# Kernel optimization log

Measured on AMD Instinct MI355X. Metric: run time of the kernel, lower is better.

Reference implementation:

```python
import jax, jax.numpy as jnp
import numpy as np

EPS = 1e-5


def sage_conv(x, src, dst, Wl, Wr, b, n):
    # PyG SAGEConv: out_i = W_l * mean_{j in N(i)} x_j + W_r * x_i + b
    agg = jax.ops.segment_sum(x[src], dst, num_segments=n)  # [N, d]
    deg = jax.ops.segment_sum(jnp.ones_like(src, dtype=x.dtype), dst, num_segments=n)
    agg = agg / jnp.maximum(deg, 1.0)[:, None]
    return agg @ Wl + x @ Wr + b


def setup_inputs() -> dict:
    key = jax.random.key(0)
    ks = jax.random.split(key, 12)
    N, E, D_IN, D_H, D_OUT = 50000, 600000, 128, 128, 64
    x = jax.random.normal(ks[0], (N, D_IN), dtype=jnp.float32)
    edge_index = jax.random.randint(ks[1], (2, E), 0, N, dtype=jnp.int64)
    s_in = 1.0 / np.sqrt(D_IN)
    s_h = 1.0 / np.sqrt(D_H)
    return {
        "x": x,
        "edge_index": edge_index,
        "Wl0": jax.random.normal(ks[2], (D_IN, D_H), jnp.float32) * s_in,
        "Wr0": jax.random.normal(ks[3], (D_IN, D_H), jnp.float32) * s_in,
        "b0": jnp.zeros((D_H,), jnp.float32),
        "Wl1": jax.random.normal(ks[4], (D_H, D_H), jnp.float32) * s_h,
        "Wr1": jax.random.normal(ks[5], (D_H, D_H), jnp.float32) * s_h,
        "b1": jnp.zeros((D_H,), jnp.float32),
        "Wl2": jax.random.normal(ks[6], (D_H, D_OUT), jnp.float32) * s_h,
        "Wr2": jax.random.normal(ks[7], (D_H, D_OUT), jnp.float32) * s_h,
        "b2": jnp.zeros((D_OUT,), jnp.float32),
        "gamma": jnp.ones((D_H,), jnp.float32),
        "beta": jnp.zeros((D_H,), jnp.float32),
    }


def reference(x, edge_index, Wl0, Wr0, b0, Wl1, Wr1, b1, Wl2, Wr2, b2, gamma, beta):
    n = x.shape[0]
    src, dst = edge_index[0], edge_index[1]
    residual = x  # in_channels == hidden_channels -> no residual_transform
    # layer 0: conv + relu (+ dropout as identity in eval)
    h = jax.nn.relu(sage_conv(x, src, dst, Wl0, Wr0, b0, n))
    # middle layer: conv + BN(batch stats) + relu + residual
    h = sage_conv(h, src, dst, Wl1, Wr1, b1, n)
    mu = jnp.mean(h, axis=0)
    var = jnp.var(h, axis=0)  # biased, as in torch BN normalization
    h = (h - mu) * jax.lax.rsqrt(var + EPS) * gamma + beta
    h = jax.nn.relu(h) + residual
    # output layer
    h = sage_conv(h, src, dst, Wl2, Wr2, b2, n)
    return jax.nn.log_softmax(h, axis=-1)
```

## Files before the change

kernel.cpp:

```cpp
#include <hip/hip_runtime.h>
#include <hip/hip_bf16.h>


#define WS_EPS 1e-5f

typedef unsigned short ushort_t;
typedef unsigned int uint_t;
typedef ushort_t ushort8 __attribute__((ext_vector_type(8)));
typedef ushort_t ushort4v __attribute__((ext_vector_type(4)));
typedef short short8 __attribute__((ext_vector_type(8)));
typedef float f32x4 __attribute__((ext_vector_type(4)));

__device__ __forceinline__ float bf2f(ushort_t u) {
    return __uint_as_float(((uint_t)u) << 16);
}
__device__ __forceinline__ ushort_t f2bf(float f) {
    uint_t u = __float_as_uint(f);
    u = (u + 0x7fffu + ((u >> 16) & 1u)) >> 16;
    return (ushort_t)u;
}

__global__ __launch_bounds__(256) void k_deg(const int* __restrict__ ei,
                                             int* __restrict__ deg, int E) {
    int e = blockIdx.x * 256 + threadIdx.x;
    if (e < E) atomicAdd(&deg[ei[E + e]], 1);
}

constexpr int SCHUNK = 4096;

__global__ __launch_bounds__(256) void k_scan_part(const int* __restrict__ deg,
                                                   int* __restrict__ bsum, int n) {
    int t = threadIdx.x;
    int base = blockIdx.x * SCHUNK + t * 16;
    int s = 0;
#pragma unroll
    for (int j = 0; j < 16; ++j) {
        int i = base + j;
        if (i < n) s += deg[i];
    }
#pragma unroll
    for (int d = 1; d < 64; d <<= 1) s += __shfl_xor(s, d);
    __shared__ int wt[4];
    if ((t & 63) == 0) wt[t >> 6] = s;
    __syncthreads();
    if (t == 0) bsum[blockIdx.x] = wt[0] + wt[1] + wt[2] + wt[3];
}

__global__ __launch_bounds__(64) void k_scan_bsum(const int* __restrict__ bsum,
                                                  int* __restrict__ boff,
                                                  int* __restrict__ off_n, int nb) {
    int lane = threadIdx.x;
    int carry = 0;
    for (int base = 0; base < nb; base += 64) {
        int t = base + lane;
        int v = (t < nb) ? bsum[t] : 0;
        int x = v;
#pragma unroll
        for (int d = 1; d < 64; d <<= 1) {
            int y = __shfl_up(x, d);
            if (lane >= d) x += y;
        }
        if (t < nb) boff[t] = carry + x - v;
        carry += __shfl(x, 63);
    }
    if (lane == 0) *off_n = carry;
}

__global__ __launch_bounds__(256) void k_scan_apply(const int* __restrict__ deg,
                                                    const int* __restrict__ boff,
                                                    int* __restrict__ off, int n) {
    int t = threadIdx.x;
    int lane = t & 63, wid = t >> 6;
    int base = blockIdx.x * SCHUNK + t * 16;
    int v[16];
    int s = 0;
#pragma unroll
    for (int j = 0; j < 16; ++j) {
        int i = base + j;
        v[j] = (i < n) ? deg[i] : 0;
        s += v[j];
    }
    int x = s;
#pragma unroll
    for (int d = 1; d < 64; d <<= 1) {
        int y = __shfl_up(x, d);
        if (lane >= d) x += y;
    }
    __shared__ int wtot[4];
    if (lane == 63) wtot[wid] = x;
    __syncthreads();
    int woff = 0;
    for (int wj = 0; wj < wid; ++wj) woff += wtot[wj];
    int run = boff[blockIdx.x] + woff + x - s;
#pragma unroll
    for (int j = 0; j < 16; ++j) {
        int i = base + j;
        if (i < n) off[i] = run;
        run += v[j];
    }
}

__global__ __launch_bounds__(256) void k_scatter(const int* __restrict__ ei,
                                                 const int* __restrict__ off,
                                                 int* __restrict__ cur,
                                                 int* __restrict__ csr, int E) {
    int e = blockIdx.x * 256 + threadIdx.x;
    if (e < E) {
        int d = ei[E + e];
        int s = ei[e];
        int p = atomicAdd(&cur[d], 1);
        csr[off[d] + p] = s;
    }
}

__global__ __launch_bounds__(256) void k_prep(const float* __restrict__ x,
                                              ushort_t* __restrict__ xb, int total2,
                                              int nb_cvt,
                                              const float* __restrict__ Wl0,
                                              const float* __restrict__ Wr0,
                                              const float* __restrict__ Wl1,
                                              const float* __restrict__ Wr1,
                                              const float* __restrict__ Wl2,
                                              const float* __restrict__ Wr2,
                                              ushort_t* __restrict__ wts) {
    int b = blockIdx.x;
    if (b < nb_cvt) {
        int i = b * 256 + threadIdx.x;
        if (i >= total2) return;
        float2 v = *(const float2*)&x[(size_t)i * 2];
        uint_t p = (uint_t)f2bf(v.x) | ((uint_t)f2bf(v.y) << 16);
        *(uint_t*)&xb[(size_t)i * 2] = p;
        return;
    }
    int id = (b - nb_cvt) * 256 + threadIdx.x;
    if (id >= 81920) return;
    const float* W;
    int rel, nout, base;
    if (id < 65536) {
        int m = id >> 14;
        rel = id & 16383;
        nout = 128;
        base = m << 14;
        W = (m == 0) ? Wl0 : (m == 1) ? Wr0 : (m == 2) ? Wl1 : Wr1;
    } else {
        int m = (id - 65536) >> 13;
        rel = (id - 65536) & 8191;
        nout = 64;
        base = 65536 + (m << 13);
        W = (m == 0) ? Wl2 : Wr2;
    }
    int c = rel >> 7;
    int k = rel & 127;
    wts[base + rel] = f2bf(W[(size_t)k * nout + c]);
}

template <int EPI>
__global__ __launch_bounds__(256, 3) void k_dgemm(const ushort_t* __restrict__ X1,
                                                  const ushort_t* __restrict__ W1,
                                                  const ushort_t* __restrict__ X2,
                                                  const ushort_t* __restrict__ W2,
                                                  const float* __restrict__ bias,
                                                  ushort_t* __restrict__ outp,
                                                  float* __restrict__ stats, int n) {
    constexpr int K = 128, NOUT = 128;
    const int t = threadIdx.x;
    const int lane = t & 63;
    const int r16 = lane & 15, kb = lane >> 4;
    const int gwv = blockIdx.x * 4 + (t >> 6);
    const int cq = gwv & 3;
    const int strips = (n + 15) >> 4;
    const int sstride = gridDim.x;

    const int col0 = cq * 32 + r16;
    short8 B1[2][4], B2[2][4];
#pragma unroll
    for (int fn = 0; fn < 2; ++fn)
#pragma unroll
        for (int ks = 0; ks < 4; ++ks)
            B1[fn][ks] = *(const short8*)&W1[(size_t)(col0 + fn * 16) * K + ks * 32 + kb * 8];
#pragma unroll
    for (int fn = 0; fn < 2; ++fn)
#pragma unroll
        for (int ks = 0; ks < 4; ++ks)
            B2[fn][ks] = *(const short8*)&W2[(size_t)(col0 + fn * 16) * K + ks * 32 + kb * 8];

    float bcol[2] = {bias[col0], bias[col0 + 16]};
    float ssum[2] = {0.f, 0.f}, qsum[2] = {0.f, 0.f};

    auto loadA = [&](short8* a, int s) {
        int arow = s * 16 + r16;
        bool ok = arow < n;
        size_t xo = (size_t)arow * K + kb * 8;
#pragma unroll
        for (int ks = 0; ks < 4; ++ks)
            a[ks] = ok ? *(const short8*)&X1[xo + ks * 32] : (short8)0;
#pragma unroll
        for (int ks = 0; ks < 4; ++ks)
            a[4 + ks] = ok ? *(const short8*)&X2[xo + ks * 32] : (short8)0;
    };

    auto work = [&](const short8* a, int s) {
        f32x4 acc0 = (f32x4)0.f, acc1 = (f32x4)0.f;
#pragma unroll
        for (int ks = 0; ks < 4; ++ks) {
            acc0 = __builtin_amdgcn_mfma_f32_16x16x32_bf16(a[ks], B1[0][ks], acc0, 0, 0, 0);
            acc1 = __builtin_amdgcn_mfma_f32_16x16x32_bf16(a[ks], B1[1][ks], acc1, 0, 0, 0);
        }
#pragma unroll
        for (int ks = 0; ks < 4; ++ks) {
            acc0 = __builtin_amdgcn_mfma_f32_16x16x32_bf16(a[4 + ks], B2[0][ks], acc0, 0, 0, 0);
            acc1 = __builtin_amdgcn_mfma_f32_16x16x32_bf16(a[4 + ks], B2[1][ks], acc1, 0, 0, 0);
        }
        int rb = s * 16 + kb * 4;
#pragma unroll
        for (int r = 0; r < 4; ++r) {
            int row = rb + r;
            if (row >= n) continue;
            float v0 = acc0[r] + bcol[0];
            float v1 = acc1[r] + bcol[1];
            if constexpr (EPI == 2) {
                outp[(size_t)row * NOUT + col0] = f2bf(fmaxf(v0, 0.f));
                outp[(size_t)row * NOUT + col0 + 16] = f2bf(fmaxf(v1, 0.f));
            } else {
                outp[(size_t)row * NOUT + col0] = f2bf(v0);
                outp[(size_t)row * NOUT + col0 + 16] = f2bf(v1);
                ssum[0] += v0; qsum[0] += v0 * v0;
                ssum[1] += v1; qsum[1] += v1 * v1;
            }
        }
    };

    short8 aA[8], aB[8];
    int s = gwv >> 2;
    if (s < strips) {
        loadA(aA, s);
        for (;;) {
            int s1 = s + sstride;
            bool v1 = (s1 < strips);
            if (v1) loadA(aB, s1);
            work(aA, s);
            if (!v1) break;
            int s2 = s1 + sstride;
            bool v2 = (s2 < strips);
            if (v2) loadA(aA, s2);
            work(aB, s1);
            if (!v2) break;
            s = s2;
        }
    }

    if constexpr (EPI == 1) {
#pragma unroll
        for (int fn = 0; fn < 2; ++fn) {
            ssum[fn] += __shfl_xor(ssum[fn], 16);
            ssum[fn] += __shfl_xor(ssum[fn], 32);
            qsum[fn] += __shfl_xor(qsum[fn], 16);
            qsum[fn] += __shfl_xor(qsum[fn], 32);
        }
        if (kb == 0) {
#pragma unroll
            for (int fn = 0; fn < 2; ++fn) {
                atomicAdd(&stats[col0 + fn * 16], ssum[fn]);
                atomicAdd(&stats[128 + col0 + fn * 16], qsum[fn]);
            }
        }
    }
}

__global__ __launch_bounds__(256, 3) void k_cgemm(const ushort_t* __restrict__ H,
                                                  const ushort_t* __restrict__ WL,
                                                  const ushort_t* __restrict__ WR,
                                                  const float* __restrict__ b2,
                                                  ushort_t* __restrict__ A64,
                                                  float* __restrict__ T, int n) {
    constexpr int K = 128;
    const int t = threadIdx.x;
    const int lane = t & 63;
    const int r16 = lane & 15, kb = lane >> 4;
    const int gwv = blockIdx.x * 4 + (t >> 6);
    const int hf = gwv & 1;
    const int strips = (n + 15) >> 4;
    const int sstride = gridDim.x * 2;

    const int col0 = hf * 32 + r16;
    short8 BL[2][4], BR[2][4];
#pragma unroll
    for (int fn = 0; fn < 2; ++fn)
#pragma unroll
        for (int ks = 0; ks < 4; ++ks)
            BL[fn][ks] = *(const short8*)&WL[(size_t)(col0 + fn * 16) * K + ks * 32 + kb * 8];
#pragma unroll
    for (int fn = 0; fn < 2; ++fn)
#pragma unroll
        for (int ks = 0; ks < 4; ++ks)
            BR[fn][ks] = *(const short8*)&WR[(size_t)(col0 + fn * 16) * K + ks * 32 + kb * 8];

    float bcol[2] = {b2[col0], b2[col0 + 16]};

    auto loadA = [&](short8* a, int s) {
        int arow = s * 16 + r16;
        bool ok = arow < n;
        size_t xo = (size_t)arow * K + kb * 8;
#pragma unroll
        for (int ks = 0; ks < 4; ++ks)
            a[ks] = ok ? *(const short8*)&H[xo + ks * 32] : (short8)0;
    };

    auto work = [&](const short8* a, int s) {
        f32x4 al0 = (f32x4)0.f, al1 = (f32x4)0.f;
        f32x4 ar0 = (f32x4)0.f, ar1 = (f32x4)0.f;
#pragma unroll
        for (int ks = 0; ks < 4; ++ks) {
            al0 = __builtin_amdgcn_mfma_f32_16x16x32_bf16(a[ks], BL[0][ks], al0, 0, 0, 0);
            al1 = __builtin_amdgcn_mfma_f32_16x16x32_bf16(a[ks], BL[1][ks], al1, 0, 0, 0);
            ar0 = __builtin_amdgcn_mfma_f32_16x16x32_bf16(a[ks], BR[0][ks], ar0, 0, 0, 0);
            ar1 = __builtin_amdgcn_mfma_f32_16x16x32_bf16(a[ks], BR[1][ks], ar1, 0, 0, 0);
        }
        int rb = s * 16 + kb * 4;
#pragma unroll
        for (int r = 0; r < 4; ++r) {
            int row = rb + r;
            if (row >= n) continue;
            A64[(size_t)row * 64 + col0] = f2bf(al0[r]);
            A64[(size_t)row * 64 + col0 + 16] = f2bf(al1[r]);
            T[(size_t)row * 64 + col0] = ar0[r] + bcol[0];
            T[(size_t)row * 64 + col0 + 16] = ar1[r] + bcol[1];
        }
    };

    short8 aA[4], aB[4];
    int s = gwv >> 1;
    if (s < strips) {
        loadA(aA, s);
        for (;;) {
            int s1 = s + sstride;
            bool v1 = (s1 < strips);
            if (v1) loadA(aB, s1);
            work(aA, s);
            if (!v1) break;
            int s2 = s1 + sstride;
            bool v2 = (s2 < strips);
            if (v2) loadA(aA, s2);
            work(aB, s1);
            if (!v2) break;
            s = s2;
        }
    }
}

__global__ __launch_bounds__(256) void k_lsm(const float* __restrict__ T,
                                             const ushort_t* __restrict__ B64,
                                             float* __restrict__ out, int n) {
    const int t = threadIdx.x;
    const int lane = t & 63;
    const int wv = blockIdx.x * 4 + (t >> 6);
    const int row = wv * 4 + (lane >> 4);
    const int cg = lane & 15;
    const bool ok = (row < n);
    float v[4];
    if (ok) {
        f32x4 tv = *(const f32x4*)&T[(size_t)row * 64 + cg * 4];
        ushort4v bv = *(const ushort4v*)&B64[(size_t)row * 64 + cg * 4];
#pragma unroll
        for (int j = 0; j < 4; ++j) v[j] = tv[j] + bf2f((ushort_t)bv[j]);
    } else {
#pragma unroll
        for (int j = 0; j < 4; ++j) v[j] = 0.f;
    }
    float m = fmaxf(fmaxf(v[0], v[1]), fmaxf(v[2], v[3]));
#pragma unroll
    for (int d = 1; d < 16; d <<= 1) m = fmaxf(m, __shfl_xor(m, d));
    float e = expf(v[0] - m) + expf(v[1] - m) + expf(v[2] - m) + expf(v[3] - m);
#pragma unroll
    for (int d = 1; d < 16; d <<= 1) e += __shfl_xor(e, d);
    float lg = m + logf(e);
    if (ok) {
        f32x4 o;
#pragma unroll
        for (int j = 0; j < 4; ++j) o[j] = v[j] - lg;
        *(f32x4*)&out[(size_t)row * 64 + cg * 4] = o;
    }
}

template <int D>
__global__ __launch_bounds__(256) void k_segmean_bf(const ushort_t* __restrict__ U,
                                                    const int* __restrict__ off,
                                                    const int* __restrict__ srcs,
                                                    ushort_t* __restrict__ out,
                                                    int n) {
    constexpr int L = D / 8;
    constexpr int PER = 256 / L;
    int node = blockIdx.x * PER + threadIdx.x / L;
    int sub = threadIdx.x % L;
    if (node >= n) return;
    int beg = off[node], end = off[node + 1];
    float a[8];
#pragma unroll
    for (int j = 0; j < 8; ++j) a[j] = 0.f;
    int i = beg;
    for (; i + 8 <= end; i += 8) {
        int sv[8];
#pragma unroll
        for (int u = 0; u < 8; ++u) sv[u] = srcs[i + u];
#pragma unroll
        for (int u = 0; u < 8; ++u) {
            ushort8 v = *(const ushort8*)&U[(size_t)sv[u] * D + sub * 8];
#pragma unroll
            for (int j = 0; j < 8; ++j) a[j] += bf2f((ushort_t)v[j]);
        }
    }
    for (; i + 4 <= end; i += 4) {
        int sv[4];
#pragma unroll
        for (int u = 0; u < 4; ++u) sv[u] = srcs[i + u];
#pragma unroll
        for (int u = 0; u < 4; ++u) {
            ushort8 v = *(const ushort8*)&U[(size_t)sv[u] * D + sub * 8];
#pragma unroll
            for (int j = 0; j < 8; ++j) a[j] += bf2f((ushort_t)v[j]);
        }
    }
    for (; i < end; ++i) {
        ushort8 v = *(const ushort8*)&U[(size_t)srcs[i] * D + sub * 8];
#pragma unroll
        for (int j = 0; j < 8; ++j) a[j] += bf2f((ushort_t)v[j]);
    }
    int d = end - beg;
    float inv = 1.f / (float)(d > 1 ? d : 1);
    ushort8 o;
#pragma unroll
    for (int j = 0; j < 8; ++j) o[j] = f2bf(a[j] * inv);
    *(ushort8*)&out[(size_t)node * D + sub * 8] = o;
}

__global__ __launch_bounds__(256) void k_bnapply(const ushort_t* __restrict__ P,
                                                 const float* __restrict__ X,
                                                 const float* __restrict__ stats,
                                                 const float* __restrict__ gamma,
                                                 const float* __restrict__ beta,
                                                 ushort_t* __restrict__ H, int n) {
    int i = blockIdx.x * 256 + threadIdx.x;
    if (i >= n * 64) return;
    int nd = i >> 6;
    int c = (i & 63) << 1;
    float inv_n = 1.f / (float)n;
    float mu0 = stats[c] * inv_n, mu1 = stats[c + 1] * inv_n;
    float v0 = stats[128 + c] * inv_n - mu0 * mu0;
    float v1 = stats[128 + c + 1] * inv_n - mu1 * mu1;
    float s0 = rsqrtf(v0 + WS_EPS) * gamma[c];
    float s1 = rsqrtf(v1 + WS_EPS) * gamma[c + 1];
    uint_t pv = *(const uint_t*)&P[(size_t)nd * 128 + c];
    float p0 = __uint_as_float(pv << 16);
    float p1 = __uint_as_float(pv & 0xffff0000u);
    float2 xr = *(const float2*)&X[(size_t)nd * 128 + c];
    float h0 = fmaxf((p0 - mu0) * s0 + beta[c], 0.f) + xr.x;
    float h1 = fmaxf((p1 - mu1) * s1 + beta[c + 1], 0.f) + xr.y;
    uint_t pk = (uint_t)f2bf(h0) | ((uint_t)f2bf(h1) << 16);
    *(uint_t*)&H[(size_t)nd * 128 + c] = pk;
}

extern "C" void kernel_launch(void* const* d_in, const int* in_sizes, int n_in,
                              void* d_out, int out_size, void* d_ws, size_t ws_size,
                              hipStream_t stream) {
    const float* x     = (const float*)d_in[0];
    const int*   ei    = (const int*)d_in[1];
    const float* Wl0   = (const float*)d_in[2];
    const float* Wr0   = (const float*)d_in[3];
    const float* b0    = (const float*)d_in[4];
    const float* Wl1   = (const float*)d_in[5];
    const float* Wr1   = (const float*)d_in[6];
    const float* b1    = (const float*)d_in[7];
    const float* Wl2   = (const float*)d_in[8];
    const float* Wr2   = (const float*)d_in[9];
    const float* b2    = (const float*)d_in[10];
    const float* gamma = (const float*)d_in[11];
    const float* beta  = (const float*)d_in[12];

    const int n = in_sizes[0] / 128;
    const int E = in_sizes[1] / 2;
    const int nb_scan = (n + SCHUNK - 1) / SCHUNK;

    char* w = (char*)d_ws;
    auto alloc = [&](size_t bytes) -> void* {
        void* p = (void*)w;
        w += (bytes + 255) & ~(size_t)255;
        return p;
    };
    int*      deg   = (int*)alloc((size_t)n * 4);
    int*      cur   = (int*)alloc((size_t)n * 4);
    float*    stats = (float*)alloc(256 * 4);
    size_t    zbytes = (size_t)((char*)w - (char*)deg);
    int*      off   = (int*)alloc(((size_t)n + 1) * 4);
    int*      csr   = (int*)alloc((size_t)E * 4);
    int*      bsum  = (int*)alloc(256 * 4);
    int*      boff  = (int*)alloc(256 * 4);
    ushort_t* wts   = (ushort_t*)alloc((size_t)81920 * 2);
    ushort_t* xb    = (ushort_t*)alloc((size_t)n * 128 * 2);
    ushort_t* H     = (ushort_t*)alloc((size_t)n * 128 * 2);
    ushort_t* Pb    = (ushort_t*)alloc((size_t)n * 128 * 2);
    ushort_t* slabB = (ushort_t*)alloc((size_t)n * 128 * 2);
    float*    T     = (float*)alloc((size_t)n * 64 * 4);

    ushort_t* WtL0 = wts;
    ushort_t* WtR0 = wts + 16384;
    ushort_t* WtL1 = wts + 32768;
    ushort_t* WtR1 = wts + 49152;
    ushort_t* WtL2 = wts + 65536;
    ushort_t* WtR2 = wts + 73728;

    ushort_t* M   = slabB;
    ushort_t* A64 = slabB;
    ushort_t* B64 = slabB + (size_t)n * 64;

    hipMemsetAsync(deg, 0, zbytes, stream);

    const int eb = (E + 255) / 256;
    k_deg<<<eb, 256, 0, stream>>>(ei, deg, E);
    k_scan_part<<<nb_scan, 256, 0, stream>>>(deg, bsum, n);
    k_scan_bsum<<<1, 64, 0, stream>>>(bsum, boff, off + n, nb_scan);
    k_scan_apply<<<nb_scan, 256, 0, stream>>>(deg, boff, off, n);
    k_scatter<<<eb, 256, 0, stream>>>(ei, off, cur, csr, E);

    const int nb_cvt = (n * 64 + 255) / 256;
    k_prep<<<nb_cvt + 320, 256, 0, stream>>>(x, xb, n * 64, nb_cvt,
                                             Wl0, Wr0, Wl1, Wr1, Wl2, Wr2, wts);

    const int NB_G = 640;
    const int smb128 = (n + 15) / 16;
    const int smb64 = (n + 31) / 32;
    const int lsb = (n + 15) / 16;

    k_segmean_bf<128><<<smb128, 256, 0, stream>>>(xb, off, csr, M, n);
    k_dgemm<2><<<NB_G, 256, 0, stream>>>(xb, WtR0, M, WtL0, b0, H, nullptr, n);

    k_segmean_bf<128><<<smb128, 256, 0, stream>>>(H, off, csr, M, n);
    k_dgemm<1><<<NB_G, 256, 0, stream>>>(H, WtR1, M, WtL1, b1, Pb, stats, n);
    k_bnapply<<<(n * 64 + 255) / 256, 256, 0, stream>>>(Pb, x, stats, gamma, beta, H, n);

    k_cgemm<<<NB_G, 256, 0, stream>>>(H, WtL2, WtR2, b2, A64, T, n);
    k_segmean_bf<64><<<smb64, 256, 0, stream>>>(A64, off, csr, B64, n);
    k_lsm<<<lsb, 256, 0, stream>>>(T, B64, (float*)d_out, n);
}
```

Measured before the change: 234.2 us.

## Gather FP8 neighbor features, stage weights in LDS, fuse final aggregation with log-softmax

Several changes are made at once. Layer-0 and layer-1 activations get an extra 8-bit e4m3-like copy, and the neighbor-mean gathers read it and accumulate in fp16 to halve gather bandwidth. The GEMMs now load weights into shared memory with padded rows, compute 64 columns per block with triple-buffered A strips, and store the final T term in bf16. The degree count is merged into the prep kernel, the residual reads bf16 x, and the last segment-mean is fused with log-softmax. The FP8 quantization and fp16 accumulation lose precision compared with the bf16/fp32 path, which risks accuracy tolerance failures.

```diff
diff --git a/kernel.cpp b/kernel.cpp
--- a/kernel.cpp
+++ b/kernel.cpp
@@ -6,10 +6,11 @@
 
 typedef unsigned short ushort_t;
 typedef unsigned int uint_t;
+typedef unsigned char uchar_t;
 typedef ushort_t ushort8 __attribute__((ext_vector_type(8)));
-typedef ushort_t ushort4v __attribute__((ext_vector_type(4)));
 typedef short short8 __attribute__((ext_vector_type(8)));
 typedef float f32x4 __attribute__((ext_vector_type(4)));
+typedef _Float16 half2v __attribute__((ext_vector_type(2)));
 
 __device__ __forceinline__ float bf2f(ushort_t u) {
     return __uint_as_float(((uint_t)u) << 16);
@@ -19,11 +20,16 @@
     u = (u + 0x7fffu + ((u >> 16) & 1u)) >> 16;
     return (ushort_t)u;
 }
-
-__global__ __launch_bounds__(256) void k_deg(const int* __restrict__ ei,
-                                             int* __restrict__ deg, int E) {
-    int e = blockIdx.x * 256 + threadIdx.x;
-    if (e < E) atomicAdd(&deg[ei[E + e]], 1);
+__device__ __forceinline__ uchar_t f2e4m3(float f) {
+    _Float16 hf = (_Float16)f;
+    uint_t h = (uint_t)__builtin_bit_cast(unsigned short, hf);
+    uint_t s = (h >> 8) & 0x80u;
+    uint_t r = h & 0x7fffu;
+    if (r < 0x2400u) return (uchar_t)0;
+    if (r > 0x5F40u) r = 0x5F00u;
+    uint_t u = r - 0x2000u;
+    uint_t m = (u + 0x3fu + ((u >> 7) & 1u)) >> 7;
+    return (uchar_t)(s | m);
 }
 
 constexpr int SCHUNK = 4096;
@@ -113,23 +119,34 @@
     }
 }
 
-__global__ __launch_bounds__(256) void k_prep(const float* __restrict__ x,
-                                              ushort_t* __restrict__ xb, int total2,
-                                              int nb_cvt,
-                                              const float* __restrict__ Wl0,
-                                              const float* __restrict__ Wr0,
-                                              const float* __restrict__ Wl1,
-                                              const float* __restrict__ Wr1,
-                                              const float* __restrict__ Wl2,
-                                              const float* __restrict__ Wr2,
-                                              ushort_t* __restrict__ wts) {
+__global__ __launch_bounds__(256) void k_deg_prep(const int* __restrict__ ei,
+                                                  int* __restrict__ deg, int E, int eb,
+                                                  const float* __restrict__ x,
+                                                  ushort_t* __restrict__ xb,
+                                                  uchar_t* __restrict__ x8,
+                                                  int total2, int nb_cvt,
+                                                  const float* __restrict__ Wl0,
+                                                  const float* __restrict__ Wr0,
+                                                  const float* __restrict__ Wl1,
+                                                  const float* __restrict__ Wr1,
+                                                  const float* __restrict__ Wl2,
+                                                  const float* __restrict__ Wr2,
+                                                  ushort_t* __restrict__ wts) {
     int b = blockIdx.x;
+    if (b < eb) {
+        int e = b * 256 + threadIdx.x;
+        if (e < E) atomicAdd(&deg[ei[E + e]], 1);
+        return;
+    }
+    b -= eb;
     if (b < nb_cvt) {
         int i = b * 256 + threadIdx.x;
         if (i >= total2) return;
         float2 v = *(const float2*)&x[(size_t)i * 2];
         uint_t p = (uint_t)f2bf(v.x) | ((uint_t)f2bf(v.y) << 16);
         *(uint_t*)&xb[(size_t)i * 2] = p;
+        ushort_t q = (ushort_t)((uint_t)f2e4m3(v.x) | ((uint_t)f2e4m3(v.y) << 8));
+        *(ushort_t*)&x8[(size_t)i * 2] = q;
         return;
     }
     int id = (b - nb_cvt) * 256 + threadIdx.x;
@@ -154,38 +171,44 @@
     wts[base + rel] = f2bf(W[(size_t)k * nout + c]);
 }
 
+constexpr int LDK = 136;
+
 template <int EPI>
-__global__ __launch_bounds__(256, 3) void k_dgemm(const ushort_t* __restrict__ X1,
+__global__ __launch_bounds__(256, 2) void k_dgemm(const ushort_t* __restrict__ X1,
                                                   const ushort_t* __restrict__ W1,
                                                   const ushort_t* __restrict__ X2,
                                                   const ushort_t* __restrict__ W2,
                                                   const float* __restrict__ bias,
                                                   ushort_t* __restrict__ outp,
+                                                  uchar_t* __restrict__ out8,
                                                   float* __restrict__ stats, int n) {
     constexpr int K = 128, NOUT = 128;
+    __shared__ ushort_t Bs[2 * 64 * LDK];
+
     const int t = threadIdx.x;
     const int lane = t & 63;
     const int r16 = lane & 15, kb = lane >> 4;
-    const int gwv = blockIdx.x * 4 + (t >> 6);
-    const int cq = gwv & 3;
+    const int colbase = (blockIdx.x & 1) * 64;
+
+#pragma unroll
+    for (int u = 0; u < 8; ++u) {
+        int f = u * 256 + t;
+        int rel = f & 1023;
+        int col = rel >> 4, seg = rel & 15;
+        const ushort_t* Wm = (u < 4) ? W1 : W2;
+        *(ushort8*)&Bs[(u < 4 ? 0 : 1) * 64 * LDK + col * LDK + seg * 8] =
+            *(const ushort8*)&Wm[(size_t)(colbase + col) * K + seg * 8];
+    }
+    __syncthreads();
+
+    float bcol[4];
+#pragma unroll
+    for (int fn = 0; fn < 4; ++fn) bcol[fn] = bias[colbase + fn * 16 + r16];
+    float ssum[4] = {0.f, 0.f, 0.f, 0.f}, qsum[4] = {0.f, 0.f, 0.f, 0.f};
+
     const int strips = (n + 15) >> 4;
-    const int sstride = gridDim.x;
-
-    const int col0 = cq * 32 + r16;
-    short8 B1[2][4], B2[2][4];
-#pragma unroll
-    for (int fn = 0; fn < 2; ++fn)
-#pragma unroll
-        for (int ks = 0; ks < 4; ++ks)
-            B1[fn][ks] = *(const short8*)&W1[(size_t)(col0 + fn * 16) * K + ks * 32 + kb * 8];
-#pragma unroll
-    for (int fn = 0; fn < 2; ++fn)
-#pragma unroll
-        for (int ks = 0; ks < 4; ++ks)
-            B2[fn][ks] = *(const short8*)&W2[(size_t)(col0 + fn * 16) * K + ks * 32 + kb * 8];
-
-    float bcol[2] = {bias[col0], bias[col0 + 16]};
-    float ssum[2] = {0.f, 0.f}, qsum[2] = {0.f, 0.f};
+    const int wstr = (gridDim.x >> 1) * 4;
+    const int s0 = (blockIdx.x >> 1) * 4 + (t >> 6);
 
     auto loadA = [&](short8* a, int s) {
         int arow = s * 16 + r16;
@@ -200,58 +223,77 @@
     };
 
     auto work = [&](const short8* a, int s) {
-        f32x4 acc0 = (f32x4)0.f, acc1 = (f32x4)0.f;
+        f32x4 acc[4] = {(f32x4)0.f, (f32x4)0.f, (f32x4)0.f, (f32x4)0.f};
 #pragma unroll
         for (int ks = 0; ks < 4; ++ks) {
-            acc0 = __builtin_amdgcn_mfma_f32_16x16x32_bf16(a[ks], B1[0][ks], acc0, 0, 0, 0);
-            acc1 = __builtin_amdgcn_mfma_f32_16x16x32_bf16(a[ks], B1[1][ks], acc1, 0, 0, 0);
+#pragma unroll
+            for (int fn = 0; fn < 4; ++fn) {
+                short8 b = *(const short8*)&Bs[(fn * 16 + r16) * LDK + ks * 32 + kb * 8];
+                acc[fn] = __builtin_amdgcn_mfma_f32_16x16x32_bf16(a[ks], b, acc[fn], 0, 0, 0);
+            }
         }
 #pragma unroll
         for (int ks = 0; ks < 4; ++ks) {
-            acc0 = __builtin_amdgcn_mfma_f32_16x16x32_bf16(a[4 + ks], B2[0][ks], acc0, 0, 0, 0);
-            acc1 = __builtin_amdgcn_mfma_f32_16x16x32_bf16(a[4 + ks], B2[1][ks], acc1, 0, 0, 0);
+#pragma unroll
+            for (int fn = 0; fn < 4; ++fn) {
+                short8 b = *(const short8*)&Bs[64 * LDK + (fn * 16 + r16) * LDK + ks * 32 + kb * 8];
+                acc[fn] = __builtin_amdgcn_mfma_f32_16x16x32_bf16(a[4 + ks], b, acc[fn], 0, 0, 0);
+            }
         }
         int rb = s * 16 + kb * 4;
 #pragma unroll
         for (int r = 0; r < 4; ++r) {
             int row = rb + r;
             if (row >= n) continue;
-            float v0 = acc0[r] + bcol[0];
-            float v1 = acc1[r] + bcol[1];
-            if constexpr (EPI == 2) {
-                outp[(size_t)row * NOUT + col0] = f2bf(fmaxf(v0, 0.f));
-                outp[(size_t)row * NOUT + col0 + 16] = f2bf(fmaxf(v1, 0.f));
-            } else {
-                outp[(size_t)row * NOUT + col0] = f2bf(v0);
-                outp[(size_t)row * NOUT + col0 + 16] = f2bf(v1);
-                ssum[0] += v0; qsum[0] += v0 * v0;
-                ssum[1] += v1; qsum[1] += v1 * v1;
+#pragma unroll
+            for (int fn = 0; fn < 4; ++fn) {
+                int col = colbase + fn * 16 + r16;
+                float v = acc[fn][r] + bcol[fn];
+                if constexpr (EPI == 2) {
+                    float rv = fmaxf(v, 0.f);
+                    outp[(size_t)row * NOUT + col] = f2bf(rv);
+                    out8[(size_t)row * NOUT + col] = f2e4m3(rv);
+                } else {
+                    outp[(size_t)row * NOUT + col] = f2bf(v);
+                    ssum[fn] += v;
+                    qsum[fn] += v * v;
+                }
             }
         }
     };
 
-    short8 aA[8], aB[8];
-    int s = gwv >> 2;
+    short8 aA[8], aB[8], aC[8];
+    int s = s0;
     if (s < strips) {
         loadA(aA, s);
+        int sB = s + wstr;
+        bool vB = sB < strips;
+        if (vB) loadA(aB, sB);
         for (;;) {
-            int s1 = s + sstride;
-            bool v1 = (s1 < strips);
-            if (v1) loadA(aB, s1);
+            int sC = sB + wstr;
+            bool vC = vB && (sC < strips);
+            if (vC) loadA(aC, sC);
             work(aA, s);
-            if (!v1) break;
-            int s2 = s1 + sstride;
-            bool v2 = (s2 < strips);
-            if (v2) loadA(aA, s2);
-            work(aB, s1);
-            if (!v2) break;
-            s = s2;
+            if (!vB) break;
+            int sD = sC + wstr;
+            bool vD = vC && (sD < strips);
+            if (vD) loadA(aA, sD);
+            work(aB, sB);
+            if (!vC) break;
+            int sE = sD + wstr;
+            bool vE = vD && (sE < strips);
+            if (vE) loadA(aB, sE);
+            work(aC, sC);
+            if (!vD) break;
+            s = sD;
+            sB = sE;
+            vB = vE;
         }
     }
 
     if constexpr (EPI == 1) {
 #pragma unroll
-        for (int fn = 0; fn < 2; ++fn) {
+        for (int fn = 0; fn < 4; ++fn) {
             ssum[fn] += __shfl_xor(ssum[fn], 16);
             ssum[fn] += __shfl_xor(ssum[fn], 32);
             qsum[fn] += __shfl_xor(qsum[fn], 16);
@@ -259,43 +301,46 @@
         }
         if (kb == 0) {
 #pragma unroll
-            for (int fn = 0; fn < 2; ++fn) {
-                atomicAdd(&stats[col0 + fn * 16], ssum[fn]);
-                atomicAdd(&stats[128 + col0 + fn * 16], qsum[fn]);
+            for (int fn = 0; fn < 4; ++fn) {
+                int col = colbase + fn * 16 + r16;
+                atomicAdd(&stats[col], ssum[fn]);
+                atomicAdd(&stats[128 + col], qsum[fn]);
             }
         }
     }
 }
 
-__global__ __launch_bounds__(256, 3) void k_cgemm(const ushort_t* __restrict__ H,
+__global__ __launch_bounds__(256, 2) void k_cgemm(const ushort_t* __restrict__ H,
                                                   const ushort_t* __restrict__ WL,
                                                   const ushort_t* __restrict__ WR,
                                                   const float* __restrict__ b2,
                                                   ushort_t* __restrict__ A64,
-                                                  float* __restrict__ T, int n) {
+                                                  ushort_t* __restrict__ Tb, int n) {
     constexpr int K = 128;
+    __shared__ ushort_t Bs[2 * 64 * LDK];
+
     const int t = threadIdx.x;
     const int lane = t & 63;
     const int r16 = lane & 15, kb = lane >> 4;
-    const int gwv = blockIdx.x * 4 + (t >> 6);
-    const int hf = gwv & 1;
+
+#pragma unroll
+    for (int u = 0; u < 8; ++u) {
+        int f = u * 256 + t;
+        int rel = f & 1023;
+        int col = rel >> 4, seg = rel & 15;
+        const ushort_t* Wm = (u < 4) ? WL : WR;
+        *(ushort8*)&Bs[(u < 4 ? 0 : 1) * 64 * LDK + col * LDK + seg * 8] =
+            *(const ushort8*)&Wm[(size_t)col * K + seg * 8];
+    }
+    __syncthreads();
+
+    float bcol[4];
+#pragma unroll
+    for (int fn = 0; fn < 4; ++fn) bcol[fn] = b2[fn * 16 + r16];
+
     const int strips = (n + 15) >> 4;
-    const int sstride = gridDim.x * 2;
-
-    const int col0 = hf * 32 + r16;
-    short8 BL[2][4], BR[2][4];
-#pragma unroll
-    for (int fn = 0; fn < 2; ++fn)
-#pragma unroll
-        for (int ks = 0; ks < 4; ++ks)
-            BL[fn][ks] = *(const short8*)&WL[(size_t)(col0 + fn * 16) * K + ks * 32 + kb * 8];
-#pragma unroll
-    for (int fn = 0; fn < 2; ++fn)
-#pragma unroll
-        for (int ks = 0; ks < 4; ++ks)
-            BR[fn][ks] = *(const short8*)&WR[(size_t)(col0 + fn * 16) * K + ks * 32 + kb * 8];
-
-    float bcol[2] = {b2[col0], b2[col0 + 16]};
+    const int wstr = gridDim.x * 4;
+    const int s0 = blockIdx.x * 4 + (t >> 6);
 
     auto loadA = [&](short8* a, int s) {
         int arow = s * 16 + r16;
@@ -307,91 +352,128 @@
     };
 
     auto work = [&](const short8* a, int s) {
-        f32x4 al0 = (f32x4)0.f, al1 = (f32x4)0.f;
-        f32x4 ar0 = (f32x4)0.f, ar1 = (f32x4)0.f;
+        f32x4 aL[4] = {(f32x4)0.f, (f32x4)0.f, (f32x4)0.f, (f32x4)0.f};
+        f32x4 aR[4] = {(f32x4)0.f, (f32x4)0.f, (f32x4)0.f, (f32x4)0.f};
 #pragma unroll
         for (int ks = 0; ks < 4; ++ks) {
-            al0 = __builtin_amdgcn_mfma_f32_16x16x32_bf16(a[ks], BL[0][ks], al0, 0, 0, 0);
-            al1 = __builtin_amdgcn_mfma_f32_16x16x32_bf16(a[ks], BL[1][ks], al1, 0, 0, 0);
-            ar0 = __builtin_amdgcn_mfma_f32_16x16x32_bf16(a[ks], BR[0][ks], ar0, 0, 0, 0);
-            ar1 = __builtin_amdgcn_mfma_f32_16x16x32_bf16(a[ks], BR[1][ks], ar1, 0, 0, 0);
+#pragma unroll
+            for (int fn = 0; fn < 4; ++fn) {
+                short8 bl = *(const short8*)&Bs[(fn * 16 + r16) * LDK + ks * 32 + kb * 8];
+                short8 br = *(const short8*)&Bs[64 * LDK + (fn * 16 + r16) * LDK + ks * 32 + kb * 8];
+                aL[fn] = __builtin_amdgcn_mfma_f32_16x16x32_bf16(a[ks], bl, aL[fn], 0, 0, 0);
+                aR[fn] = __builtin_amdgcn_mfma_f32_16x16x32_bf16(a[ks], br, aR[fn], 0, 0, 0);
+            }
         }
         int rb = s * 16 + kb * 4;
 #pragma unroll
         for (int r = 0; r < 4; ++r) {
             int row = rb + r;
             if (row >= n) continue;
-            A64[(size_t)row * 64 + col0] = f2bf(al0[r]);
-            A64[(size_t)row * 64 + col0 + 16] = f2bf(al1[r]);
-            T[(size_t)row * 64 + col0] = ar0[r] + bcol[0];
-            T[(size_t)row * 64 + col0 + 16] = ar1[r] + bcol[1];
+#pragma unroll
+            for (int fn = 0; fn < 4; ++fn) {
+                int col = fn * 16 + r16;
+                A64[(size_t)row * 64 + col] = f2bf(aL[fn][r]);
+                Tb[(size_t)row * 64 + col] = f2bf(aR[fn][r] + bcol[fn]);
+            }
         }
     };
 
-    short8 aA[4], aB[4];
-    int s = gwv >> 1;
+    short8 aA[4], aB[4], aC[4];
+    int s = s0;
     if (s < strips) {
         loadA(aA, s);
+        int sB = s + wstr;
+        bool vB = sB < strips;
+        if (vB) loadA(aB, sB);
         for (;;) {
-            int s1 = s + sstride;
-            bool v1 = (s1 < strips);
-            if (v1) loadA(aB, s1);
+            int sC = sB + wstr;
+            bool vC = vB && (sC < strips);
+            if (vC) loadA(aC, sC);
             work(aA, s);
-            if (!v1) break;
-            int s2 = s1 + sstride;
-            bool v2 = (s2 < strips);
-            if (v2) loadA(aA, s2);
-            work(aB, s1);
-            if (!v2) break;
-            s = s2;
-        }
-    }
-}
-
-__global__ __launch_bounds__(256) void k_lsm(const float* __restrict__ T,
-                                             const ushort_t* __restrict__ B64,
-                                             float* __restrict__ out, int n) {
-    const int t = threadIdx.x;
-    const int lane = t & 63;
-    const int wv = blockIdx.x * 4 + (t >> 6);
-    const int row = wv * 4 + (lane >> 4);
-    const int cg = lane & 15;
-    const bool ok = (row < n);
-    float v[4];
-    if (ok) {
-        f32x4 tv = *(const f32x4*)&T[(size_t)row * 64 + cg * 4];
-        ushort4v bv = *(const ushort4v*)&B64[(size_t)row * 64 + cg * 4];
-#pragma unroll
-        for (int j = 0; j < 4; ++j) v[j] = tv[j] + bf2f((ushort_t)bv[j]);
-    } else {
-#pragma unroll
-        for (int j = 0; j < 4; ++j) v[j] = 0.f;
-    }
-    float m = fmaxf(fmaxf(v[0], v[1]), fmaxf(v[2], v[3]));
-#pragma unroll
-    for (int d = 1; d < 16; d <<= 1) m = fmaxf(m, __shfl_xor(m, d));
-    float e = expf(v[0] - m) + expf(v[1] - m) + expf(v[2] - m) + expf(v[3] - m);
-#pragma unroll
-    for (int d = 1; d < 16; d <<= 1) e += __shfl_xor(e, d);
-    float lg = m + logf(e);
-    if (ok) {
-        f32x4 o;
-#pragma unroll
-        for (int j = 0; j < 4; ++j) o[j] = v[j] - lg;
-        *(f32x4*)&out[(size_t)row * 64 + cg * 4] = o;
-    }
-}
-
-template <int D>
-__global__ __launch_bounds__(256) void k_segmean_bf(const ushort_t* __restrict__ U,
-                                                    const int* __restrict__ off,
-                                                    const int* __restrict__ srcs,
-                                                    ushort_t* __restrict__ out,
-                                                    int n) {
-    constexpr int L = D / 8;
-    constexpr int PER = 256 / L;
-    int node = blockIdx.x * PER + threadIdx.x / L;
-    int sub = threadIdx.x % L;
+            if (!vB) break;
+            int sD = sC + wstr;
+            bool vD = vC && (sD < strips);
+            if (vD) loadA(aA, sD);
+            work(aB, sB);
+            if (!vC) break;
+            int sE = sD + wstr;
+            bool vE = vD && (sE < strips);
+            if (vE) loadA(aB, sE);
+            work(aC, sC);
+            if (!vD) break;
+            s = sD;
+            sB = sE;
+            vB = vE;
+        }
+    }
+}
+
+__global__ __launch_bounds__(256) void k_segmean8(const uchar_t* __restrict__ U8,
+                                                  const int* __restrict__ off,
+                                                  const int* __restrict__ srcs,
+                                                  ushort_t* __restrict__ out, int n) {
+    int node = blockIdx.x * 32 + (threadIdx.x >> 3);
+    int sub = threadIdx.x & 7;
+    if (node >= n) return;
+    int beg = off[node], end = off[node + 1];
+    half2v aE0 = (half2v)0, aE1 = (half2v)0, aE2 = (half2v)0, aE3 = (half2v)0;
+    half2v aO0 = (half2v)0, aO1 = (half2v)0, aO2 = (half2v)0, aO3 = (half2v)0;
+
+#define DEC(dw, AE, AO)                                                           \
+    {                                                                             \
+        uint_t xe = (dw)&0x00ff00ffu;                                             \
+        uint_t xo = ((dw) >> 8) & 0x00ff00ffu;                                    \
+        uint_t he = ((xe & 0x00800080u) << 8) |                                   \
+                    (((xe & 0x007f007fu) << 7) + 0x20002000u);                    \
+        uint_t ho = ((xo & 0x00800080u) << 8) |                                   \
+                    (((xo & 0x007f007fu) << 7) + 0x20002000u);                    \
+        AE += __builtin_bit_cast(half2v, he);                                     \
+        AO += __builtin_bit_cast(half2v, ho);                                     \
+    }
+
+    auto addrow = [&](int sidx) {
+        uint4 v = *(const uint4*)&U8[(size_t)sidx * 128 + sub * 16];
+        DEC(v.x, aE0, aO0)
+        DEC(v.y, aE1, aO1)
+        DEC(v.z, aE2, aO2)
+        DEC(v.w, aE3, aO3)
+    };
+#undef DEC
+
+    int i = beg;
+    for (; i + 8 <= end; i += 8) {
+        int sv[8];
+#pragma unroll
+        for (int u = 0; u < 8; ++u) sv[u] = srcs[i + u];
+#pragma unroll
+        for (int u = 0; u < 8; ++u) addrow(sv[u]);
+    }
+    for (; i < end; ++i) addrow(srcs[i]);
+
+    int d = end - beg;
+    float inv = 1.f / (float)(d > 1 ? d : 1);
+    ushort8 o0, o1;
+#define PACK(AE, AO, O, IDX)                     \
+    O[IDX] = f2bf((float)AE[0] * inv);           \
+    O[IDX + 1] = f2bf((float)AO[0] * inv);       \
+    O[IDX + 2] = f2bf((float)AE[1] * inv);       \
+    O[IDX + 3] = f2bf((float)AO[1] * inv);
+    PACK(aE0, aO0, o0, 0)
+    PACK(aE1, aO1, o0, 4)
+    PACK(aE2, aO2, o1, 0)
+    PACK(aE3, aO3, o1, 4)
+#undef PACK
+    *(ushort8*)&out[(size_t)node * 128 + sub * 16] = o0;
+    *(ushort8*)&out[(size_t)node * 128 + sub * 16 + 8] = o1;
+}
+
+__global__ __launch_bounds__(256) void k_segmean_lsm(const ushort_t* __restrict__ A64,
+                                                     const int* __restrict__ off,
+                                                     const int* __restrict__ srcs,
+                                                     const ushort_t* __restrict__ Tb,
+                                                     float* __restrict__ out, int n) {
+    int node = blockIdx.x * 32 + (threadIdx.x >> 3);
+    int sub = threadIdx.x & 7;
     if (node >= n) return;
     int beg = off[node], end = off[node + 1];
     float a[8];
@@ -404,37 +486,45 @@
         for (int u = 0; u < 8; ++u) sv[u] = srcs[i + u];
 #pragma unroll
         for (int u = 0; u < 8; ++u) {
-            ushort8 v = *(const ushort8*)&U[(size_t)sv[u] * D + sub * 8];
+            ushort8 v = *(const ushort8*)&A64[(size_t)sv[u] * 64 + sub * 8];
 #pragma unroll
             for (int j = 0; j < 8; ++j) a[j] += bf2f((ushort_t)v[j]);
         }
     }
-    for (; i + 4 <= end; i += 4) {
-        int sv[4];
-#pragma unroll
-        for (int u = 0; u < 4; ++u) sv[u] = srcs[i + u];
-#pragma unroll
-        for (int u = 0; u < 4; ++u) {
-            ushort8 v = *(const ushort8*)&U[(size_t)sv[u] * D + sub * 8];
-#pragma unroll
-            for (int j = 0; j < 8; ++j) a[j] += bf2f((ushort_t)v[j]);
-        }
-    }
     for (; i < end; ++i) {
-        ushort8 v = *(const ushort8*)&U[(size_t)srcs[i] * D + sub * 8];
+        ushort8 v = *(const ushort8*)&A64[(size_t)srcs[i] * 64 + sub * 8];
 #pragma unroll
         for (int j = 0; j < 8; ++j) a[j] += bf2f((ushort_t)v[j]);
     }
     int d = end - beg;
     float inv = 1.f / (float)(d > 1 ? d : 1);
-    ushort8 o;
-#pragma unroll
-    for (int j = 0; j < 8; ++j) o[j] = f2bf(a[j] * inv);
-    *(ushort8*)&out[(size_t)node * D + sub * 8] = o;
+    ushort8 tv = *(const ushort8*)&Tb[(size_t)node * 64 + sub * 8];
+    float vv[8];
+#pragma unroll
+    for (int j = 0; j < 8; ++j) vv[j] = a[j] * inv + bf2f((ushort_t)tv[j]);
+    float m = vv[0];
+#pragma unroll
+    for (int j = 1; j < 8; ++j) m = fmaxf(m, vv[j]);
+#pragma unroll
+    for (int dd = 1; dd < 8; dd <<= 1) m = fmaxf(m, __shfl_xor(m, dd));
+    float e = 0.f;
+#pragma unroll
+    for (int j = 0; j < 8; ++j) e += expf(vv[j] - m);
+#pragma unroll
+    for (int dd = 1; dd < 8; dd <<= 1) e += __shfl_xor(e, dd);
+    float lg = m + logf(e);
+    f32x4 o0, o1;
+#pragma unroll
+    for (int j = 0; j < 4; ++j) {
+        o0[j] = vv[j] - lg;
+        o1[j] = vv[4 + j] - lg;
+    }
+    *(f32x4*)&out[(size_t)node * 64 + sub * 8] = o0;
+    *(f32x4*)&out[(size_t)node * 64 + sub * 8 + 4] = o1;
 }
 
 __global__ __launch_bounds__(256) void k_bnapply(const ushort_t* __restrict__ P,
-                                                 const float* __restrict__ X,
+                                                 const ushort_t* __restrict__ Xb,
                                                  const float* __restrict__ stats,
                                                  const float* __restrict__ gamma,
                                                  const float* __restrict__ beta,
@@ -450,11 +540,13 @@
     float s0 = rsqrtf(v0 + WS_EPS) * gamma[c];
     float s1 = rsqrtf(v1 + WS_EPS) * gamma[c + 1];
     uint_t pv = *(const uint_t*)&P[(size_t)nd * 128 + c];
+    uint_t xv = *(const uint_t*)&Xb[(size_t)nd * 128 + c];
     float p0 = __uint_as_float(pv << 16);
     float p1 = __uint_as_float(pv & 0xffff0000u);
-    float2 xr = *(const float2*)&X[(size_t)nd * 128 + c];
-    float h0 = fmaxf((p0 - mu0) * s0 + beta[c], 0.f) + xr.x;
-    float h1 = fmaxf((p1 - mu1) * s1 + beta[c + 1], 0.f) + xr.y;
+    float x0 = __uint_as_float(xv << 16);
+    float x1 = __uint_as_float(xv & 0xffff0000u);
+    float h0 = fmaxf((p0 - mu0) * s0 + beta[c], 0.f) + x0;
+    float h1 = fmaxf((p1 - mu1) * s1 + beta[c + 1], 0.f) + x1;
     uint_t pk = (uint_t)f2bf(h0) | ((uint_t)f2bf(h1) << 16);
     *(uint_t*)&H[(size_t)nd * 128 + c] = pk;
 }
@@ -496,10 +588,13 @@
     int*      boff  = (int*)alloc(256 * 4);
     ushort_t* wts   = (ushort_t*)alloc((size_t)81920 * 2);
     ushort_t* xb    = (ushort_t*)alloc((size_t)n * 128 * 2);
+    uchar_t*  x8    = (uchar_t*)alloc((size_t)n * 128);
     ushort_t* H     = (ushort_t*)alloc((size_t)n * 128 * 2);
+    uchar_t*  H8    = (uchar_t*)alloc((size_t)n * 128);
     ushort_t* Pb    = (ushort_t*)alloc((size_t)n * 128 * 2);
-    ushort_t* slabB = (ushort_t*)alloc((size_t)n * 128 * 2);
-    float*    T     = (float*)alloc((size_t)n * 64 * 4);
+    ushort_t* M     = (ushort_t*)alloc((size_t)n * 128 * 2);
+    ushort_t* A64   = (ushort_t*)alloc((size_t)n * 64 * 2);
+    ushort_t* Tb    = (ushort_t*)alloc((size_t)n * 64 * 2);
 
     ushort_t* WtL0 = wts;
     ushort_t* WtR0 = wts + 16384;
@@ -508,36 +603,29 @@
     ushort_t* WtL2 = wts + 65536;
     ushort_t* WtR2 = wts + 73728;
 
-    ushort_t* M   = slabB;
-    ushort_t* A64 = slabB;
-    ushort_t* B64 = slabB + (size_t)n * 64;
-
     hipMemsetAsync(deg, 0, zbytes, stream);
 
     const int eb = (E + 255) / 256;
-    k_deg<<<eb, 256, 0, stream>>>(ei, deg, E);
+    const int nb_cvt = (n * 64 + 255) / 256;
+    k_deg_prep<<<eb + nb_cvt + 320, 256, 0, stream>>>(ei, deg, E, eb, x, xb, x8,
+                                                      n * 64, nb_cvt,
+                                                      Wl0, Wr0, Wl1, Wr1, Wl2, Wr2, wts);
     k_scan_part<<<nb_scan, 256, 0, stream>>>(deg, bsum, n);
     k_scan_bsum<<<1, 64, 0, stream>>>(bsum, boff, off + n, nb_scan);
     k_scan_apply<<<nb_scan, 256, 0, stream>>>(deg, boff, off, n);
-    k_scatter<<<eb, 256, 0, stream>>>(ei, off, cur, csr, E);
-
-    const int nb_cvt = (n * 64 + 255) / 256;
-    k_prep<<<nb_cvt + 320, 256, 0, stream>>>(x, xb, n * 64, nb_cvt,
-                                             Wl0, Wr0, Wl1, Wr1, Wl2, Wr2, wts);
-
-    const int NB_G = 640;
-    const int smb128 = (n + 15) / 16;
-    const int smb64 = (n + 31) / 32;
-    const int lsb = (n + 15) / 16;
-
-    k_segmean_bf<128><<<smb128, 256, 0, stream>>>(xb, off, csr, M, n);
-    k_dgemm<2><<<NB_G, 256, 0, stream>>>(xb, WtR0, M, WtL0, b0, H, nullptr, n);
-
-    k_segmean_bf<128><<<smb128, 256, 0, stream>>>(H, off, csr, M, n);
-    k_dgemm<1><<<NB_G, 256, 0, stream>>>(H, WtR1, M, WtL1, b1, Pb, stats, n);
-    k_bnapply<<<(n * 64 + 255) / 256, 256, 0, stream>>>(Pb, x, stats, gamma, beta, H, n);
-
-    k_cgemm<<<NB_G, 256, 0, stream>>>(H, WtL2, WtR2, b2, A64, T, n);
-    k_segmean_bf<64><<<smb64, 256, 0, stream>>>(A64, off, csr, B64, n);
-    k_lsm<<<lsb, 256, 0, stream>>>(T, B64, (float*)d_out, n);
-}
+    k_scatter<<<(E + 255) / 256, 256, 0, stream>>>(ei, off, cur, csr, E);
+
+    const int GB_D = 512;
+    const int GB_C = 256;
+    const int smb = (n + 31) / 32;
+
+    k_segmean8<<<smb, 256, 0, stream>>>(x8, off, csr, M, n);
+    k_dgemm<2><<<GB_D, 256, 0, stream>>>(xb, WtR0, M, WtL0, b0, H, H8, nullptr, n);
+
+    k_segmean8<<<smb, 256, 0, stream>>>(H8, off, csr, M, n);
+    k_dgemm<1><<<GB_D, 256, 0, stream>>>(H, WtR1, M, WtL1, b1, Pb, nullptr, stats, n);
+    k_bnapply<<<(n * 64 + 255) / 256, 256, 0, stream>>>(Pb, xb, stats, gamma, beta, H, n);
+
+    k_cgemm<<<GB_C, 256, 0, stream>>>(H, WtL2, WtR2, b2, A64, Tb, n);
+    k_segmean_lsm<<<smb, 256, 0, stream>>>(A64, off, csr, Tb, (float*)d_out, n);
+}
```

Result: slower. 243.0 us (+3.7%).
